# Optimization experiments

Measured on AMD Instinct MI355X. Metric: run time of the kernel, lower is better.

Reference implementation:

```python
import jax, jax.numpy as jnp
import numpy as np

B, T, D, H = 4, 2048, 2048, 16
DH = D // H

def setup_inputs() -> dict:
    key = jax.random.key(0)
    ks = jax.random.split(key, 9)
    s = 1.0 / np.sqrt(D)
    return {
        "x": jax.random.normal(ks[0], (B, T, D), dtype=jnp.float32),
        "Wq": jax.random.uniform(ks[1], (D, D), jnp.float32, -s, s),
        "bq": jax.random.uniform(ks[2], (D,), jnp.float32, -s, s),
        "Wk": jax.random.uniform(ks[3], (D, D), jnp.float32, -s, s),
        "bk": jax.random.uniform(ks[4], (D,), jnp.float32, -s, s),
        "Wv": jax.random.uniform(ks[5], (D, D), jnp.float32, -s, s),
        "bv": jax.random.uniform(ks[6], (D,), jnp.float32, -s, s),
        "Wo": jax.random.uniform(ks[7], (D, D), jnp.float32, -s, s),
        "bo": jax.random.uniform(ks[8], (D,), jnp.float32, -s, s),
    }

def reference(x, Wq, bq, Wk, bk, Wv, bv, Wo, bo):
    # projections: [B,T,D] -> [B,H,T,DH]
    def split_heads(y):
        return y.reshape(B, T, H, DH).transpose(0, 2, 1, 3)
    q = split_heads(x @ Wq + bq)
    k = split_heads(x @ Wk + bk)
    v = split_heads(x @ Wv + bv)
    scale = DH ** -0.5
    scores = jnp.einsum('bhtd,bhsd->bhts', q, k) * scale  # [B,H,T,T]
    causal = jnp.tril(jnp.ones((T, T), dtype=bool))
    scores = jnp.where(causal[None, None], scores, -jnp.inf)
    weights = jax.nn.softmax(scores, axis=-1)
    out = jnp.einsum('bhts,bhsd->bhtd', weights, v)  # [B,H,T,DH]
    out = out.transpose(0, 2, 1, 3).reshape(B, T, D)
    return out @ Wo + bo
```

## Files before the change

### kernel.cpp

```cpp
#include <hip/hip_runtime.h>
#include <hip/hip_bf16.h>

#define B_  4
#define T_  2048
#define D_  2048
#define H_  16
#define DH_ 128

typedef __attribute__((ext_vector_type(4))) float f32x4;
typedef __attribute__((ext_vector_type(8))) short short8;
typedef __attribute__((ext_vector_type(4))) _Float16 half4;

__device__ __forceinline__ ushort f2bf(float f) {
    unsigned int u = __builtin_bit_cast(unsigned int, f);
    u += 0x7fffu + ((u >> 16) & 1u);
    return (ushort)(u >> 16);
}
__device__ __forceinline__ ushort f2h(float f) {
    return (ushort)(__builtin_bit_cast(unsigned int, __builtin_amdgcn_cvt_pkrtz(f, f)) & 0xffffu);
}

__device__ __forceinline__ void glds16(const void* g, void* l) {
    __builtin_amdgcn_global_load_lds(
        (const __attribute__((address_space(1))) unsigned int*)g,
        (__attribute__((address_space(3))) unsigned int*)l, 16, 0, 0);
}

__global__ void cast_f32_bf16(const float* __restrict__ x, ushort* __restrict__ xb, int n) {
    int i = (blockIdx.x * 256 + threadIdx.x) * 4;
    if (i < n) {
        float4 v = *(const float4*)(x + i);
        ushort4 o;
        o.x = f2bf(v.x); o.y = f2bf(v.y); o.z = f2bf(v.z); o.w = f2bf(v.w);
        *(ushort4*)(xb + i) = o;
    }
}

__global__ void transpose_cast4(
    const float* __restrict__ W0, const float* __restrict__ W1,
    const float* __restrict__ W2, const float* __restrict__ W3,
    ushort* __restrict__ T0, ushort* __restrict__ T1,
    ushort* __restrict__ T2, ushort* __restrict__ T3)
{
    const int z = blockIdx.z;
    const float* W = (z == 0) ? W0 : (z == 1) ? W1 : (z == 2) ? W2 : W3;
    ushort* Wt     = (z == 0) ? T0 : (z == 1) ? T1 : (z == 2) ? T2 : T3;
    __shared__ float tile[32][33];
    int tx = threadIdx.x, ty = threadIdx.y;
    int n0 = blockIdx.x * 32, k0 = blockIdx.y * 32;
#pragma unroll
    for (int i = 0; i < 4; i++)
        tile[ty + i * 8][tx] = W[(size_t)(k0 + ty + i * 8) * D_ + n0 + tx];
    __syncthreads();
#pragma unroll
    for (int i = 0; i < 4; i++)
        Wt[(size_t)(n0 + ty + i * 8) * D_ + k0 + tx] = f2bf(tile[tx][ty + i * 8]);
}

__global__ __launch_bounds__(256, 3) void gemm_qkv(
    const ushort* __restrict__ A,
    const ushort* __restrict__ Wq, const ushort* __restrict__ Wk, const ushort* __restrict__ Wv,
    const float* __restrict__ bq, const float* __restrict__ bk, const float* __restrict__ bv,
    ushort* __restrict__ Qb, ushort* __restrict__ Kb, ushort* __restrict__ Vtb,
    float qscale)
{
    extern __shared__ char smem[];
    uint4* sA = (uint4*)smem;
    uint4* sB = (uint4*)(smem + 8192);

    const int tid  = threadIdx.x;
    const int sel  = blockIdx.x >> 4;
    const int row0 = blockIdx.y * 128, col0 = (blockIdx.x & 15) * 128;
    const ushort* Bt = (sel == 0) ? Wq : (sel == 1) ? Wk : Wv;
    const float* bias = (sel == 0) ? bq : (sel == 1) ? bk : bv;
    const float oscale = (sel == 0) ? qscale : 1.0f;
    const int K = D_, N = D_;

    const int mA = tid >> 2, g = tid & 3;
    const int gc = g ^ ((mA >> 2) & 3);
    const ushort* pa0 = A  + (size_t)(row0 + mA) * K + gc * 8;
    const ushort* pb0 = Bt + (size_t)(col0 + mA) * K + gc * 8;

    const int lane = tid & 63, w = tid >> 6;
    const int l15 = lane & 15, quad = lane >> 4;
    const int wm = w & 1, wn = w >> 1;
    const int csel = quad ^ ((l15 >> 2) & 3);
    int aoff[4], boff[4];
#pragma unroll
    for (int mt = 0; mt < 4; mt++) aoff[mt] = (wm * 64 + mt * 16 + l15) * 4 + csel;
#pragma unroll
    for (int nt = 0; nt < 4; nt++) boff[nt] = (wn * 64 + nt * 16 + l15) * 4 + csel;

    f32x4 acc[4][4] = {};

    const int kIter = K >> 5;
    for (int kt = 0; kt < kIter; ++kt) {
        if (kt) __syncthreads();
        glds16(pa0 + kt * 32,                     sA + tid);
        glds16(pa0 + kt * 32 + (size_t)64 * K,    sA + tid + 256);
        glds16(pb0 + kt * 32,                     sB + tid);
        glds16(pb0 + kt * 32 + (size_t)64 * K,    sB + tid + 256);
        __syncthreads();
        short8 af[4], bfr[4];
#pragma unroll
        for (int mt = 0; mt < 4; mt++) af[mt]  = __builtin_bit_cast(short8, sA[aoff[mt]]);
#pragma unroll
        for (int nt = 0; nt < 4; nt++) bfr[nt] = __builtin_bit_cast(short8, sB[boff[nt]]);
#pragma unroll
        for (int mt = 0; mt < 4; mt++)
#pragma unroll
            for (int nt = 0; nt < 4; nt++)
                acc[mt][nt] = __builtin_amdgcn_mfma_f32_16x16x32_bf16(af[mt], bfr[nt], acc[mt][nt], 0, 0, 0);
    }

    if (sel < 2) {
        ushort* Cout = (sel == 0) ? Qb : Kb;
#pragma unroll
        for (int nt = 0; nt < 4; nt++) {
            int col = col0 + wn * 64 + nt * 16 + l15;
            float bb = bias[col];
#pragma unroll
            for (int mt = 0; mt < 4; mt++) {
                int rowb = row0 + wm * 64 + mt * 16 + quad * 4;
#pragma unroll
                for (int r = 0; r < 4; ++r)
                    Cout[(size_t)(rowb + r) * N + col] = f2bf((acc[mt][nt][r] + bb) * oscale);
            }
        }
    } else {
        __syncthreads();
        ushort* tr = (ushort*)smem;
#pragma unroll
        for (int nt = 0; nt < 4; nt++) {
            int cl = wn * 64 + nt * 16 + l15;
            float bb = bias[col0 + cl];
#pragma unroll
            for (int mt = 0; mt < 4; mt++) {
                int rl = wm * 64 + mt * 16 + quad * 4;
#pragma unroll
                for (int r = 0; r < 4; ++r)
                    tr[cl * 136 + rl + r] = f2h(acc[mt][nt][r] + bb);
            }
        }
        __syncthreads();
        int b = row0 >> 11, t0 = row0 & (T_ - 1), h = col0 >> 7;
        for (int idx = tid; idx < 2048; idx += 256) {
            int dh = idx >> 4, c = idx & 15;
            uint4 v = *(const uint4*)(tr + dh * 136 + c * 8);
            *(uint4*)(Vtb + (size_t)((b * H_ + h) * DH_ + dh) * T_ + t0 + c * 8) = v;
        }
    }
}

__global__ __launch_bounds__(256, 3) void gemm_bt_f32(
    const ushort* __restrict__ A, const ushort* __restrict__ Bt,
    const float* __restrict__ bias, float* __restrict__ Cout,
    int M, int N, int K)
{
    extern __shared__ char smem[];
    uint4* sA = (uint4*)smem;
    uint4* sB = (uint4*)(smem + 8192);

    const int tid  = threadIdx.x;
    const int row0 = blockIdx.y * 128, col0 = blockIdx.x * 128;

    const int mA = tid >> 2, g = tid & 3;
    const int gc = g ^ ((mA >> 2) & 3);
    const ushort* pa0 = A  + (size_t)(row0 + mA) * K + gc * 8;
    const ushort* pb0 = Bt + (size_t)(col0 + mA) * K + gc * 8;

    const int lane = tid & 63, w = tid >> 6;
    const int l15 = lane & 15, quad = lane >> 4;
    const int wm = w & 1, wn = w >> 1;
    const int csel = quad ^ ((l15 >> 2) & 3);
    int aoff[4], boff[4];
#pragma unroll
    for (int mt = 0; mt < 4; mt++) aoff[mt] = (wm * 64 + mt * 16 + l15) * 4 + csel;
#pragma unroll
    for (int nt = 0; nt < 4; nt++) boff[nt] = (wn * 64 + nt * 16 + l15) * 4 + csel;

    f32x4 acc[4][4] = {};

    const int kIter = K >> 5;
    for (int kt = 0; kt < kIter; ++kt) {
        if (kt) __syncthreads();
        glds16(pa0 + kt * 32,                     sA + tid);
        glds16(pa0 + kt * 32 + (size_t)64 * K,    sA + tid + 256);
        glds16(pb0 + kt * 32,                     sB + tid);
        glds16(pb0 + kt * 32 + (size_t)64 * K,    sB + tid + 256);
        __syncthreads();
        short8 af[4], bfr[4];
#pragma unroll
        for (int mt = 0; mt < 4; mt++) af[mt]  = __builtin_bit_cast(short8, sA[aoff[mt]]);
#pragma unroll
        for (int nt = 0; nt < 4; nt++) bfr[nt] = __builtin_bit_cast(short8, sB[boff[nt]]);
#pragma unroll
        for (int mt = 0; mt < 4; mt++)
#pragma unroll
            for (int nt = 0; nt < 4; nt++)
                acc[mt][nt] = __builtin_amdgcn_mfma_f32_16x16x32_bf16(af[mt], bfr[nt], acc[mt][nt], 0, 0, 0);
    }

#pragma unroll
    for (int nt = 0; nt < 4; nt++) {
        int col = col0 + wn * 64 + nt * 16 + l15;
        float bb = bias[col];
#pragma unroll
        for (int mt = 0; mt < 4; mt++) {
            int rowb = row0 + wm * 64 + mt * 16 + quad * 4;
#pragma unroll
            for (int r = 0; r < 4; ++r)
                Cout[(size_t)(rowb + r) * N + col] = acc[mt][nt][r] + bb;
        }
    }
}

__global__ __launch_bounds__(256, 3) void attn_kernel(
    const ushort* __restrict__ Q, const ushort* __restrict__ K,
    const ushort* __restrict__ Vt, ushort* __restrict__ O)
{
    __shared__ __align__(16) char smem[49152];
    uint4*  kS = (uint4*)smem;
    ushort* vS = (ushort*)(smem + 16384);

    const int tid = threadIdx.x;
    const int bid = blockIdx.x;
    const int slot = bid >> 3;
    const int g = (bid & 7) + 8 * (slot >> 4);
    const int qx = slot & 15;
    const int b = g >> 4, h = g & 15;

    const int lane = tid & 63, w = tid >> 6, l15 = lane & 15, quad = lane >> 4;

    const int krow = tid >> 4;
    const int kchunk = (tid & 15) ^ (krow & 7);
    const ushort* kg = K + ((size_t)(b * T_) + krow) * D_ + h * DH_ + kchunk * 8;

    const int vdh = tid >> 3;
    const int vslot = (tid & 7) ^ (vdh & 7);
    const ushort* vg = Vt + ((size_t)((b * H_ + h) * DH_) + vdh) * T_ + vslot * 8;
    char* vdst = smem + 16384 + tid * 16;

    const int qts[2] = { qx, 31 - qx };

    for (int e = 0; e < 2; ++e) {
        const int qt = qts[e], q0 = qt * 64;
        const int qbase = q0 + w * 16;

        short8 aq[4];
        {
            const ushort* qp = Q + ((size_t)(b * T_) + qbase + l15) * D_ + h * DH_ + quad * 8;
#pragma unroll
            for (int ks = 0; ks < 4; ++ks)
                aq[ks] = __builtin_bit_cast(short8, *(const uint4*)(qp + ks * 32));
        }

        f32x4 accO[8] = {};
        float mrow = -INFINITY, lrow = 0.f;

        __syncthreads();
#pragma unroll
        for (int j = 0; j < 4; ++j) glds16(kg + (size_t)j * 16 * D_, kS + j * 256 + tid);
#pragma unroll
        for (int j = 0; j < 4; ++j) glds16(vg + (size_t)j * 32 * T_, vdst + j * 4096);

        for (int i = 0; i <= qt; ++i) {
            const int s0 = i * 64;
            const bool diag = (i == qt);
            const int stMax = diag ? (w + 1) : 4;

            __syncthreads();

            f32x4 sT[4] = {};
#pragma unroll
            for (int ks = 0; ks < 4; ++ks)
#pragma unroll
                for (int st = 0; st < 4; ++st)
                    if (st < stMax) {
                        int row = st * 16 + l15;
                        short8 ak = __builtin_bit_cast(short8, kS[row * 16 + ((ks * 4 + quad) ^ (row & 7))]);
                        sT[st] = __builtin_amdgcn_mfma_f32_16x16x32_bf16(ak, aq[ks], sT[st], 0, 0, 0);
                    }

            __syncthreads();

            if (i < qt) {
                const ushort* kp = kg + (size_t)(s0 + 64) * D_;
#pragma unroll
                for (int j = 0; j < 4; ++j) glds16(kp + (size_t)j * 16 * D_, kS + j * 256 + tid);
                const ushort* vp = vg + s0 + 64;
                char* vd = vdst + (((i + 1) & 1) << 14);
#pragma unroll
                for (int j = 0; j < 4; ++j) glds16(vp + (size_t)j * 32 * T_, vd + j * 4096);
            }

            if (diag) {
                const int q = qbase + l15;
                const int st = stMax - 1;
#pragma unroll
                for (int r = 0; r < 4; ++r)
                    if (s0 + st * 16 + quad * 4 + r > q) sT[st][r] = -INFINITY;
            }

            float rmax = -INFINITY;
#pragma unroll
            for (int st = 0; st < 4; ++st)
                if (st < stMax)
#pragma unroll
                    for (int r = 0; r < 4; ++r) rmax = fmaxf(rmax, sT[st][r]);
            rmax = fmaxf(rmax, __shfl_xor(rmax, 16));
            rmax = fmaxf(rmax, __shfl_xor(rmax, 32));
            if (!__all(rmax <= mrow + 8.0f)) {
                float mnew  = fmaxf(mrow, rmax);
                float alpha = __builtin_amdgcn_exp2f(mrow - mnew);
                mrow = mnew;
                lrow *= alpha;
#pragma unroll
                for (int nt = 0; nt < 8; ++nt)
#pragma unroll
                    for (int r = 0; r < 4; ++r) accO[nt][r] *= alpha;
            }

            float psum = 0.f;
            half4 pb[4];
#pragma unroll
            for (int st = 0; st < 4; ++st)
                if (st < stMax) {
                    float p0 = __builtin_amdgcn_exp2f(sT[st][0] - mrow);
                    float p1 = __builtin_amdgcn_exp2f(sT[st][1] - mrow);
                    float p2 = __builtin_amdgcn_exp2f(sT[st][2] - mrow);
                    float p3 = __builtin_amdgcn_exp2f(sT[st][3] - mrow);
                    psum += (p0 + p1) + (p2 + p3);
                    uint2 u;
                    u.x = __builtin_bit_cast(unsigned int, __builtin_amdgcn_cvt_pkrtz(p0, p1));
                    u.y = __builtin_bit_cast(unsigned int, __builtin_amdgcn_cvt_pkrtz(p2, p3));
                    pb[st] = __builtin_bit_cast(half4, u);
                }
            psum += __shfl_xor(psum, 16);
            psum += __shfl_xor(psum, 32);
            lrow += psum;

            const ushort* vb = vS + ((i & 1) << 13);
#pragma unroll
            for (int st = 0; st < 4; ++st)
                if (st < stMax) {
                    const int s8 = st * 4 + quad;
                    const int off = (((s8 >> 1) ^ (l15 & 7)) << 3) + ((s8 & 1) << 2);
#pragma unroll
                    for (int nt = 0; nt < 8; ++nt) {
                        int dh = nt * 16 + l15;
                        half4 vf = *(const half4*)(vb + dh * 64 + off);
                        accO[nt] = __builtin_amdgcn_mfma_f32_16x16x16f16(vf, pb[st], accO[nt], 0, 0, 0);
                    }
                }
        }

        __syncthreads();
        ushort* eT = (ushort*)smem + w * 2176;
        float inv = 1.0f / lrow;
#pragma unroll
        for (int nt = 0; nt < 8; ++nt) {
            int dh = nt * 16 + quad * 4;
#pragma unroll
            for (int r = 0; r < 4; ++r)
                eT[l15 * 136 + dh + r] = f2bf(accO[nt][r] * inv);
        }
        for (int idx = lane; idx < 256; idx += 64) {
            int row = idx >> 4, c = idx & 15;
            uint4 v = *(const uint4*)(eT + row * 136 + c * 8);
            *(uint4*)(O + ((size_t)(b * T_) + q0 + w * 16 + row) * D_ + h * DH_ + c * 8) = v;
        }
    }
}

extern "C" void kernel_launch(void* const* d_in, const int* in_sizes, int n_in,
                              void* d_out, int out_size, void* d_ws, size_t ws_size,
                              hipStream_t stream) {
    const float* x  = (const float*)d_in[0];
    const float* Wq = (const float*)d_in[1];
    const float* bq = (const float*)d_in[2];
    const float* Wk = (const float*)d_in[3];
    const float* bk = (const float*)d_in[4];
    const float* Wv = (const float*)d_in[5];
    const float* bv = (const float*)d_in[6];
    const float* Wo = (const float*)d_in[7];
    const float* bo = (const float*)d_in[8];

    char* ws = (char*)d_ws;
    const size_t MB = 1u << 20;
    ushort* xb  = (ushort*)(ws);
    ushort* Wqt = (ushort*)(ws + 32 * MB);
    ushort* Wkt = (ushort*)(ws + 40 * MB);
    ushort* Wvt = (ushort*)(ws + 48 * MB);
    ushort* Wot = (ushort*)(ws + 56 * MB);
    ushort* Qb  = (ushort*)(ws + 64 * MB);
    ushort* Kb  = (ushort*)(ws + 96 * MB);
    ushort* Vtb = (ushort*)(ws + 128 * MB);
    ushort* Ob  = (ushort*)(ws + 160 * MB);

    const int M = B_ * T_;
    const float qscale = (float)(0.08838834764831845 * 1.4426950408889634);

    cast_f32_bf16<<<(M * D_) / 1024, 256, 0, stream>>>(x, xb, M * D_);
    dim3 tb(32, 8), tg(D_ / 32, D_ / 32, 4);
    transpose_cast4<<<tg, tb, 0, stream>>>(Wq, Wk, Wv, Wo, Wqt, Wkt, Wvt, Wot);

    gemm_qkv<<<dim3(48, M / 128), 256, 34816, stream>>>(
        xb, Wqt, Wkt, Wvt, bq, bk, bv, Qb, Kb, Vtb, qscale);

    attn_kernel<<<dim3(1024), 256, 0, stream>>>(Qb, Kb, Vtb, Ob);

    gemm_bt_f32<<<dim3(D_ / 128, M / 128), 256, 16384, stream>>>(
        Ob, Wot, bo, (float*)d_out, M, D_, D_);
}
```

Measured before the change: 639.1 us.

## Process both paired query tiles in one pass sharing K/V tile loads

Instead of processing the two paired query tiles (qx and 31-qx) one after another, each reloading K/V, the block now walks the KV sequence once and computes both tiles against every staged K/V tile, skipping tile A once it passes its causal limit. This roughly halves K/V global loads per block and the number of barriers, and gives more independent MFMA work between syncs. It also adds s_setprio around the MFMA sections. The cost is doubled accumulator and Q register state (two 8x f32x4 accumulators), which raises register pressure and may reduce occupancy or cause spills.

Result: slower. 977.4 us (+52.9%).

```diff
diff --git a/kernel.cpp b/kernel.cpp
--- a/kernel.cpp
+++ b/kernel.cpp
@@ -241,122 +241,153 @@
     const ushort* vg = Vt + ((size_t)((b * H_ + h) * DH_) + vdh) * T_ + vslot * 8;
     char* vdst = smem + 16384 + tid * 16;
 
-    const int qts[2] = { qx, 31 - qx };
-
-    for (int e = 0; e < 2; ++e) {
-        const int qt = qts[e], q0 = qt * 64;
-        const int qbase = q0 + w * 16;
-
-        short8 aq[4];
+    const int qtA = qx, qtB = 31 - qx;
+    const int nT = qtB + 1;
+
+    short8 aqA[4], aqB[4];
+    {
+        const ushort* qpA = Q + ((size_t)(b * T_) + qtA * 64 + w * 16 + l15) * D_ + h * DH_ + quad * 8;
+        const ushort* qpB = Q + ((size_t)(b * T_) + qtB * 64 + w * 16 + l15) * D_ + h * DH_ + quad * 8;
+#pragma unroll
+        for (int ks = 0; ks < 4; ++ks) {
+            aqA[ks] = __builtin_bit_cast(short8, *(const uint4*)(qpA + ks * 32));
+            aqB[ks] = __builtin_bit_cast(short8, *(const uint4*)(qpB + ks * 32));
+        }
+    }
+
+    f32x4 accA[8] = {}, accB[8] = {};
+    float mA = -INFINITY, lA = 0.f;
+    float mB = -INFINITY, lB = 0.f;
+
+    auto qkt = [&](short8 (&aq)[4], int stMax, f32x4 (&sT)[4]) {
+        __builtin_amdgcn_s_setprio(1);
+#pragma unroll
+        for (int ks = 0; ks < 4; ++ks)
+#pragma unroll
+            for (int st = 0; st < 4; ++st)
+                if (st < stMax) {
+                    int row = st * 16 + l15;
+                    short8 ak = __builtin_bit_cast(short8, kS[row * 16 + ((ks * 4 + quad) ^ (row & 7))]);
+                    sT[st] = __builtin_amdgcn_mfma_f32_16x16x32_bf16(ak, aq[ks], sT[st], 0, 0, 0);
+                }
+        __builtin_amdgcn_s_setprio(0);
+    };
+
+    auto softmax = [&](f32x4 (&sT)[4], int stMax, float& mrow, float& lrow,
+                       f32x4 (&accO)[8], half4 (&pb)[4]) {
+        float rmax = -INFINITY;
+#pragma unroll
+        for (int st = 0; st < 4; ++st)
+            if (st < stMax)
+#pragma unroll
+                for (int r = 0; r < 4; ++r) rmax = fmaxf(rmax, sT[st][r]);
+        rmax = fmaxf(rmax, __shfl_xor(rmax, 16));
+        rmax = fmaxf(rmax, __shfl_xor(rmax, 32));
+        if (!__all(rmax <= mrow + 8.0f)) {
+            float mnew  = fmaxf(mrow, rmax);
+            float alpha = __builtin_amdgcn_exp2f(mrow - mnew);
+            mrow = mnew;
+            lrow *= alpha;
+#pragma unroll
+            for (int nt = 0; nt < 8; ++nt)
+#pragma unroll
+                for (int r = 0; r < 4; ++r) accO[nt][r] *= alpha;
+        }
+        float psum = 0.f;
+#pragma unroll
+        for (int st = 0; st < 4; ++st)
+            if (st < stMax) {
+                float p0 = __builtin_amdgcn_exp2f(sT[st][0] - mrow);
+                float p1 = __builtin_amdgcn_exp2f(sT[st][1] - mrow);
+                float p2 = __builtin_amdgcn_exp2f(sT[st][2] - mrow);
+                float p3 = __builtin_amdgcn_exp2f(sT[st][3] - mrow);
+                psum += (p0 + p1) + (p2 + p3);
+                uint2 u;
+                u.x = __builtin_bit_cast(unsigned int, __builtin_amdgcn_cvt_pkrtz(p0, p1));
+                u.y = __builtin_bit_cast(unsigned int, __builtin_amdgcn_cvt_pkrtz(p2, p3));
+                pb[st] = __builtin_bit_cast(half4, u);
+            }
+        psum += __shfl_xor(psum, 16);
+        psum += __shfl_xor(psum, 32);
+        lrow += psum;
+    };
+
+    auto pv = [&](const ushort* vb, half4 (&pb)[4], int stMax, f32x4 (&accO)[8]) {
+#pragma unroll
+        for (int st = 0; st < 4; ++st)
+            if (st < stMax) {
+                const int s8 = st * 4 + quad;
+                const int off = (((s8 >> 1) ^ (l15 & 7)) << 3) + ((s8 & 1) << 2);
+#pragma unroll
+                for (int nt = 0; nt < 8; ++nt) {
+                    int dh = nt * 16 + l15;
+                    half4 vf = *(const half4*)(vb + dh * 64 + off);
+                    accO[nt] = __builtin_amdgcn_mfma_f32_16x16x16f16(vf, pb[st], accO[nt], 0, 0, 0);
+                }
+            }
+    };
+
+#pragma unroll
+    for (int j = 0; j < 4; ++j) glds16(kg + (size_t)j * 16 * D_, kS + j * 256 + tid);
+#pragma unroll
+    for (int j = 0; j < 4; ++j) glds16(vg + (size_t)j * 32 * T_, vdst + j * 4096);
+
+    for (int i = 0; i < nT; ++i) {
+        const int s0 = i * 64;
+        const bool actA = (i <= qtA);
+        const int stMaxA = (i == qtA) ? (w + 1) : 4;
+        const int stMaxB = (i == qtB) ? (w + 1) : 4;
+
+        __syncthreads();
+
+        half4 pbA[4], pbB[4];
         {
-            const ushort* qp = Q + ((size_t)(b * T_) + qbase + l15) * D_ + h * DH_ + quad * 8;
-#pragma unroll
-            for (int ks = 0; ks < 4; ++ks)
-                aq[ks] = __builtin_bit_cast(short8, *(const uint4*)(qp + ks * 32));
-        }
-
-        f32x4 accO[8] = {};
-        float mrow = -INFINITY, lrow = 0.f;
-
-        __syncthreads();
-#pragma unroll
-        for (int j = 0; j < 4; ++j) glds16(kg + (size_t)j * 16 * D_, kS + j * 256 + tid);
-#pragma unroll
-        for (int j = 0; j < 4; ++j) glds16(vg + (size_t)j * 32 * T_, vdst + j * 4096);
-
-        for (int i = 0; i <= qt; ++i) {
-            const int s0 = i * 64;
-            const bool diag = (i == qt);
-            const int stMax = diag ? (w + 1) : 4;
-
-            __syncthreads();
-
             f32x4 sT[4] = {};
-#pragma unroll
-            for (int ks = 0; ks < 4; ++ks)
-#pragma unroll
-                for (int st = 0; st < 4; ++st)
-                    if (st < stMax) {
-                        int row = st * 16 + l15;
-                        short8 ak = __builtin_bit_cast(short8, kS[row * 16 + ((ks * 4 + quad) ^ (row & 7))]);
-                        sT[st] = __builtin_amdgcn_mfma_f32_16x16x32_bf16(ak, aq[ks], sT[st], 0, 0, 0);
-                    }
-
-            __syncthreads();
-
-            if (i < qt) {
-                const ushort* kp = kg + (size_t)(s0 + 64) * D_;
-#pragma unroll
-                for (int j = 0; j < 4; ++j) glds16(kp + (size_t)j * 16 * D_, kS + j * 256 + tid);
-                const ushort* vp = vg + s0 + 64;
-                char* vd = vdst + (((i + 1) & 1) << 14);
-#pragma unroll
-                for (int j = 0; j < 4; ++j) glds16(vp + (size_t)j * 32 * T_, vd + j * 4096);
-            }
-
-            if (diag) {
-                const int q = qbase + l15;
-                const int st = stMax - 1;
+            qkt(aqB, stMaxB, sT);
+            if (i == qtB) {
+                const int q = qtB * 64 + w * 16 + l15;
+                const int st = stMaxB - 1;
 #pragma unroll
                 for (int r = 0; r < 4; ++r)
                     if (s0 + st * 16 + quad * 4 + r > q) sT[st][r] = -INFINITY;
             }
-
-            float rmax = -INFINITY;
-#pragma unroll
-            for (int st = 0; st < 4; ++st)
-                if (st < stMax)
-#pragma unroll
-                    for (int r = 0; r < 4; ++r) rmax = fmaxf(rmax, sT[st][r]);
-            rmax = fmaxf(rmax, __shfl_xor(rmax, 16));
-            rmax = fmaxf(rmax, __shfl_xor(rmax, 32));
-            if (!__all(rmax <= mrow + 8.0f)) {
-                float mnew  = fmaxf(mrow, rmax);
-                float alpha = __builtin_amdgcn_exp2f(mrow - mnew);
-                mrow = mnew;
-                lrow *= alpha;
-#pragma unroll
-                for (int nt = 0; nt < 8; ++nt)
-#pragma unroll
-                    for (int r = 0; r < 4; ++r) accO[nt][r] *= alpha;
-            }
-
-            float psum = 0.f;
-            half4 pb[4];
-#pragma unroll
-            for (int st = 0; st < 4; ++st)
-                if (st < stMax) {
-                    float p0 = __builtin_amdgcn_exp2f(sT[st][0] - mrow);
-                    float p1 = __builtin_amdgcn_exp2f(sT[st][1] - mrow);
-                    float p2 = __builtin_amdgcn_exp2f(sT[st][2] - mrow);
-                    float p3 = __builtin_amdgcn_exp2f(sT[st][3] - mrow);
-                    psum += (p0 + p1) + (p2 + p3);
-                    uint2 u;
-                    u.x = __builtin_bit_cast(unsigned int, __builtin_amdgcn_cvt_pkrtz(p0, p1));
-                    u.y = __builtin_bit_cast(unsigned int, __builtin_amdgcn_cvt_pkrtz(p2, p3));
-                    pb[st] = __builtin_bit_cast(half4, u);
-                }
-            psum += __shfl_xor(psum, 16);
-            psum += __shfl_xor(psum, 32);
-            lrow += psum;
-
-            const ushort* vb = vS + ((i & 1) << 13);
-#pragma unroll
-            for (int st = 0; st < 4; ++st)
-                if (st < stMax) {
-                    const int s8 = st * 4 + quad;
-                    const int off = (((s8 >> 1) ^ (l15 & 7)) << 3) + ((s8 & 1) << 2);
-#pragma unroll
-                    for (int nt = 0; nt < 8; ++nt) {
-                        int dh = nt * 16 + l15;
-                        half4 vf = *(const half4*)(vb + dh * 64 + off);
-                        accO[nt] = __builtin_amdgcn_mfma_f32_16x16x16f16(vf, pb[st], accO[nt], 0, 0, 0);
-                    }
-                }
-        }
-
-        __syncthreads();
-        ushort* eT = (ushort*)smem + w * 2176;
+            softmax(sT, stMaxB, mB, lB, accB, pbB);
+        }
+        if (actA) {
+            f32x4 sT[4] = {};
+            qkt(aqA, stMaxA, sT);
+            if (i == qtA) {
+                const int q = qtA * 64 + w * 16 + l15;
+                const int st = stMaxA - 1;
+#pragma unroll
+                for (int r = 0; r < 4; ++r)
+                    if (s0 + st * 16 + quad * 4 + r > q) sT[st][r] = -INFINITY;
+            }
+            softmax(sT, stMaxA, mA, lA, accA, pbA);
+        }
+
+        __syncthreads();
+
+        if (i + 1 < nT) {
+            const ushort* kp = kg + (size_t)(s0 + 64) * D_;
+#pragma unroll
+            for (int j = 0; j < 4; ++j) glds16(kp + (size_t)j * 16 * D_, kS + j * 256 + tid);
+            const ushort* vp = vg + s0 + 64;
+            char* vd = vdst + (((i + 1) & 1) << 14);
+#pragma unroll
+            for (int j = 0; j < 4; ++j) glds16(vp + (size_t)j * 32 * T_, vd + j * 4096);
+        }
+
+        const ushort* vb = vS + ((i & 1) << 13);
+        __builtin_amdgcn_s_setprio(1);
+        pv(vb, pbB, stMaxB, accB);
+        if (actA) pv(vb, pbA, stMaxA, accA);
+        __builtin_amdgcn_s_setprio(0);
+    }
+
+    __syncthreads();
+    ushort* eT = (ushort*)smem + w * 2176;
+    auto epi = [&](f32x4 (&accO)[8], float lrow, int q0) {
         float inv = 1.0f / lrow;
 #pragma unroll
         for (int nt = 0; nt < 8; ++nt) {
@@ -370,7 +401,9 @@
             uint4 v = *(const uint4*)(eT + row * 136 + c * 8);
             *(uint4*)(O + ((size_t)(b * T_) + q0 + w * 16 + row) * D_ + h * DH_ + c * 8) = v;
         }
-    }
+    };
+    epi(accA, lA, qtA * 64);
+    epi(accB, lB, qtB * 64);
 }
 
 extern "C" void kernel_launch(void* const* d_in, const int* in_sizes, int n_in,
```
